# Kernel optimization log

Hardware: AMD Instinct MI355X
Metric: run time of the kernel (lower is better)

Reference implementation:

```python
import jax, jax.numpy as jnp
import numpy as np

B, C, D, K = 65536, 128, 32, 10
EPS = 1e-12


def setup_inputs() -> dict:
    key = jax.random.key(0)
    k1, k2, k3, k4 = jax.random.split(key, 4)
    data = jax.random.normal(k1, (B, D), dtype=jnp.float32)
    mu = jax.random.normal(k2, (C, D), dtype=jnp.float32)
    # S_inv must be symmetric positive definite (inverse covariance per cluster)
    A = 0.1 * jax.random.normal(k3, (C, D, D), dtype=jnp.float32)
    S_inv = jnp.einsum('cij,ckj->cik', A, A) + jnp.eye(D, dtype=jnp.float32)[None]
    # one-hot class assignment per cluster (int32), as stored in the module
    cls = jax.random.randint(k4, (C,), 0, K)
    cluster_labels = jax.nn.one_hot(cls, K, dtype=jnp.int32)
    return {"data": data, "mu": mu, "S_inv": S_inv, "cluster_labels": cluster_labels}


def reference(data, mu, S_inv, cluster_labels):
    # Mahalanobis distance d2[b,c] = (z_b - mu_c)^T S_inv_c (z_b - mu_c),
    # expanded to avoid a [B, C, D] diff tensor.
    zz = data[:, :, None] * data[:, None, :]            # [B, D, D]
    t1 = jnp.einsum('bde,cde->bc', zz, S_inv)           # z' Sinv z
    Sm = jnp.einsum('cde,ce->cd', S_inv, mu)            # [C, D]
    t2 = data @ Sm.T                                    # z' Sinv mu  [B, C]
    t3 = jnp.einsum('cd,cd->c', mu, Sm)                 # mu' Sinv mu [C]
    d2 = t1 - 2.0 * t2 + t3[None, :]                    # [B, C]
    Gamma = jnp.exp(-0.5 * d2)                          # Gaussian activation
    # defuzzify_batch: normalize activations, project through one-hot labels
    norm_gamma = Gamma / (jnp.sum(Gamma, axis=1, keepdims=True) + EPS)
    label_scores = norm_gamma @ cluster_labels.astype(jnp.float32)  # [B, K]
    preds = jnp.argmax(label_scores, axis=1)
    clusters = jnp.argmax(Gamma, axis=1)
    return label_scores, preds, clusters
```

## Files before the change

### kernel.cpp

```cpp
#include <hip/hip_runtime.h>
#include <cmath>

#define B_N 65536
#define C_N 128
#define D_N 32
#define K_N 10
#define EPS_F 1e-12f
#define SCALE_F (-0.72134752044448169f)

#define NKK 45
#define QFRAG_N (4 * NKK * 64 * 8)

typedef _Float16 f16x8 __attribute__((ext_vector_type(8)));
typedef float    f32x16 __attribute__((ext_vector_type(16)));

static constexpr int WDT[NKK] = {
    0,0,0,0,0,  2,2,2,2,  4,4,4,4,  6,6,6,6,  8,8,8,8,
    10,10,10, 12,12,12, 14,14,14, 16,16,16,
    18,18, 20,20, 22,22, 24,24, 26, 28, 30, 32};
static constexpr int WET[NKK] = {
    0,8,16,24,32,  2,10,18,26,  4,12,20,28,  6,14,22,30,  8,16,24,32,
    10,18,26, 12,20,28, 14,22,30, 16,24,32,
    18,26, 20,28, 22,30, 24,32, 26, 28, 30, 32};

__global__ __launch_bounds__(256) void k_prep_sm(const float* __restrict__ S,
                                                 const float* __restrict__ mu,
                                                 float* __restrict__ Sm) {
    int t = blockIdx.x * 256 + threadIdx.x;
    int c = t >> 5;
    int d = t & 31;
    const float* Sr = S + (size_t)c * (D_N * D_N) + (size_t)d * D_N;
    const float* mr = mu + (size_t)c * D_N;
    float a0 = 0.f, a1 = 0.f, a2 = 0.f, a3 = 0.f;
#pragma unroll
    for (int e = 0; e < D_N; e += 4) {
        a0 = fmaf(Sr[e + 0], mr[e + 0], a0);
        a1 = fmaf(Sr[e + 1], mr[e + 1], a1);
        a2 = fmaf(Sr[e + 2], mr[e + 2], a2);
        a3 = fmaf(Sr[e + 3], mr[e + 3], a3);
    }
    Sm[t] = (a0 + a1) + (a2 + a3);
}

__global__ __launch_bounds__(128) void k_prep_misc(const float* __restrict__ mu,
                                                   const float* __restrict__ Sm,
                                                   const int* __restrict__ onehot,
                                                   float* __restrict__ t3,
                                                   int* __restrict__ cls) {
    int c = threadIdx.x;
    const float* mr = mu + (size_t)c * D_N;
    const float* sr = Sm + (size_t)c * D_N;
    float a = 0.f;
#pragma unroll
    for (int d = 0; d < D_N; ++d) a = fmaf(mr[d], sr[d], a);
    t3[c] = a;
    int cl = 0;
#pragma unroll
    for (int k = 0; k < K_N; ++k)
        if (onehot[c * K_N + k] != 0) cl = k;
    cls[c] = cl;
}

__global__ __launch_bounds__(256) void k_packfrag(const float* __restrict__ S,
                                                  const float* __restrict__ Sm,
                                                  const float* __restrict__ t3,
                                                  _Float16* __restrict__ Qh,
                                                  _Float16* __restrict__ Ql) {
    int t = blockIdx.x * 256 + threadIdx.x;
    if (t >= QFRAG_N) return;
    int j    = t & 7;
    int lane = (t >> 3) & 63;
    int rest = t >> 9;
    int kk   = rest % NKK;
    int ct   = rest / NKK;
    int r = 0, base = 0;
    for (;;) {
        int w = (40 - 2 * r) >> 3;
        if (kk < base + w) break;
        base += w; ++r;
    }
    int e0 = 2 * r + 8 * (kk - base);
    int d  = 2 * r + (lane >> 5);
    int e  = e0 + j;
    int c  = ct * 32 + (lane & 31);
    float q = 0.f;
    if (d <= e && e <= 32) {
        float v;
        if (e < 32)      v = S[(size_t)c * (D_N * D_N) + d * D_N + e] * (d == e ? 1.f : 2.f);
        else if (d < 32) v = -2.f * Sm[c * D_N + d];
        else             v = t3[c];
        q = SCALE_F * v;
    }
    _Float16 h = (_Float16)q;
    Qh[t] = h;
    Ql[t] = (_Float16)(q - (float)h);
}

__global__ __launch_bounds__(256, 2) void k_mainv3(const float* __restrict__ data,
                                                   const _Float16* __restrict__ Qhp,
                                                   const _Float16* __restrict__ Qlp,
                                                   const int* __restrict__ clsp,
                                                   float* __restrict__ out) {
    const int lane = threadIdx.x & 63;
    const int wid  = threadIdx.x >> 6;
    const int b0w  = blockIdx.x * 128 + wid * 32;
    const int col  = lane & 31;
    const bool hi  = lane >= 32;

    __shared__ int lcls[C_N];
    if (threadIdx.x < C_N) lcls[threadIdx.x] = clsp[threadIdx.x];

    float y[34];
    {
        const float4* p0 = (const float4*)(data + (size_t)(b0w + col) * D_N);
#pragma unroll
        for (int i = 0; i < 8; ++i) {
            float4 v = p0[i];
            y[4 * i + 0] = v.x; y[4 * i + 1] = v.y;
            y[4 * i + 2] = v.z; y[4 * i + 3] = v.w;
        }
        y[32] = 1.f; y[33] = 0.f;
    }
    __syncthreads();

    f32x16 acc[4];
#pragma unroll
    for (int ct = 0; ct < 4; ++ct)
#pragma unroll
        for (int g = 0; g < 16; ++g) acc[ct][g] = 0.f;

    const f16x8* QH = (const f16x8*)Qhp;
    const f16x8* QL = (const f16x8*)Qlp;

    f16x8 qh[2][4], ql[2][4];
#pragma unroll
    for (int ct = 0; ct < 4; ++ct) {
        qh[0][ct] = QH[(ct * NKK + 0) * 64 + lane];
        ql[0][ct] = QL[(ct * NKK + 0) * 64 + lane];
    }

#pragma unroll
    for (int kk = 0; kk < NKK; ++kk) {
        const int cur = kk & 1;
        const int nxt = cur ^ 1;
        if (kk + 1 < NKK) {
#pragma unroll
            for (int ct = 0; ct < 4; ++ct) {
                qh[nxt][ct] = QH[(ct * NKK + kk + 1) * 64 + lane];
                ql[nxt][ct] = QL[(ct * NKK + kk + 1) * 64 + lane];
            }
        }

        const int dA = WDT[kk];
        const int dB = dA + 1;
        const int e0 = WET[kk];
        const float yd = hi ? y[dB] : y[dA];
        f16x8 ph, pl;
#pragma unroll
        for (int j = 0; j < 8; ++j) {
            const int e = e0 + j;
            float f = (e <= 32) ? yd * y[e] : 0.f;
            _Float16 h = (_Float16)f;
            ph[j] = h;
            pl[j] = (_Float16)(f - (float)h);
        }

#pragma unroll
        for (int ct = 0; ct < 4; ++ct)
            acc[ct] = __builtin_amdgcn_mfma_f32_32x32x16_f16(qh[cur][ct], ph, acc[ct], 0, 0, 0);
#pragma unroll
        for (int ct = 0; ct < 4; ++ct)
            acc[ct] = __builtin_amdgcn_mfma_f32_32x32x16_f16(ql[cur][ct], ph, acc[ct], 0, 0, 0);
#pragma unroll
        for (int ct = 0; ct < 4; ++ct)
            acc[ct] = __builtin_amdgcn_mfma_f32_32x32x16_f16(qh[cur][ct], pl, acc[ct], 0, 0, 0);

        __builtin_amdgcn_s_barrier();
    }

    const float hoff = hi ? 4.f : 0.f;
    const int* lc = lcls + (hi ? 4 : 0);
    float sum = 0.f, gmax = -1.f, gcf = 0.f;
    float a0 = 0, a1 = 0, a2 = 0, a3 = 0, a4 = 0, a5 = 0, a6 = 0, a7 = 0, a8 = 0, a9 = 0;
#pragma unroll
    for (int ct = 0; ct < 4; ++ct) {
        float psum = 0.f;
#pragma unroll
        for (int g = 0; g < 16; ++g) {
            float v = acc[ct][g];
            float gm;
            asm("v_exp_f32 %0, %1" : "=v"(gm) : "v"(v));
            const int cbase = ct * 32 + (g & 3) + 8 * (g >> 2);
            int cl = lc[cbase];
            psum += gm;
            float cf = (float)cbase + hoff;
            if (gm > gmax) { gmax = gm; gcf = cf; }
            a0 += (cl == 0) ? gm : 0.f;
            a1 += (cl == 1) ? gm : 0.f;
            a2 += (cl == 2) ? gm : 0.f;
            a3 += (cl == 3) ? gm : 0.f;
            a4 += (cl == 4) ? gm : 0.f;
            a5 += (cl == 5) ? gm : 0.f;
            a6 += (cl == 6) ? gm : 0.f;
            a7 += (cl == 7) ? gm : 0.f;
            a8 += (cl == 8) ? gm : 0.f;
            a9 += (cl == 9) ? gm : 0.f;
        }
        sum += psum;
    }

    sum += __shfl_xor(sum, 32, 64);
    {
        float om = __shfl_xor(gmax, 32, 64);
        float oc = __shfl_xor(gcf, 32, 64);
        bool take = (om > gmax) || (om == gmax && oc < gcf);
        if (take) { gmax = om; gcf = oc; }
    }
    a0 += __shfl_xor(a0, 32, 64);
    a1 += __shfl_xor(a1, 32, 64);
    a2 += __shfl_xor(a2, 32, 64);
    a3 += __shfl_xor(a3, 32, 64);
    a4 += __shfl_xor(a4, 32, 64);
    a5 += __shfl_xor(a5, 32, 64);
    a6 += __shfl_xor(a6, 32, 64);
    a7 += __shfl_xor(a7, 32, 64);
    a8 += __shfl_xor(a8, 32, 64);
    a9 += __shfl_xor(a9, 32, 64);

    if (!hi) {
        const int b = b0w + col;
        float inv = 1.0f / (sum + EPS_F);
        float ls[K_N] = {a0 * inv, a1 * inv, a2 * inv, a3 * inv, a4 * inv,
                         a5 * inv, a6 * inv, a7 * inv, a8 * inv, a9 * inv};
        float best = -1.f;
        int bk = 0;
#pragma unroll
        for (int k = 0; k < K_N; ++k)
            if (ls[k] > best) { best = ls[k]; bk = k; }
        float2* o2 = (float2*)(out + (size_t)b * K_N);
#pragma unroll
        for (int k2 = 0; k2 < K_N / 2; ++k2)
            o2[k2] = make_float2(ls[2 * k2], ls[2 * k2 + 1]);
        out[(size_t)B_N * K_N + b] = (float)bk;
        out[(size_t)B_N * K_N + B_N + b] = gcf;
    }
}

extern "C" void kernel_launch(void* const* d_in, const int* in_sizes, int n_in,
                              void* d_out, int out_size, void* d_ws, size_t ws_size,
                              hipStream_t stream) {
    const float* data   = (const float*)d_in[0];
    const float* mu     = (const float*)d_in[1];
    const float* S      = (const float*)d_in[2];
    const int*   onehot = (const int*)d_in[3];
    float* out = (float*)d_out;

    _Float16* Qh  = (_Float16*)d_ws;
    _Float16* Ql  = Qh + QFRAG_N;
    float*    Sm  = (float*)(Ql + QFRAG_N);
    float*    t3  = Sm + C_N * D_N;
    int*      cls = (int*)(t3 + C_N);

    hipLaunchKernelGGL(k_prep_sm, dim3((C_N * D_N) / 256), dim3(256), 0, stream,
                       S, mu, Sm);
    hipLaunchKernelGGL(k_prep_misc, dim3(1), dim3(128), 0, stream,
                       mu, Sm, onehot, t3, cls);
    hipLaunchKernelGGL(k_packfrag, dim3((QFRAG_N + 255) / 256), dim3(256), 0, stream,
                       S, Sm, t3, Qh, Ql);
    hipLaunchKernelGGL(k_mainv3, dim3(B_N / 128), dim3(256), 0, stream,
                       data, Qh, Ql, cls, out);
}
```

Before: 127.3 us.

## Fuse prep kernels into one per-cluster kernel and template-unroll main loop

Merges the three preprocessing launches (Sm, t3/labels, fragment packing) into a single kernel with one block per cluster, keeping Sm and t3 in shared memory. This removes two kernel launches and the global round-trips between them. The main kernel's k-loop becomes compile-time template recursion so table lookups are constexpr, and the per-iteration s_barrier is dropped. The fused prep does only 90 active threads per block writing scalar halves, so its stores are less coalesced.

```diff
diff --git a/kernel.cpp b/kernel.cpp
--- a/kernel.cpp
+++ b/kernel.cpp
@@ -23,80 +23,119 @@
     10,18,26, 12,20,28, 14,22,30, 16,24,32,
     18,26, 20,28, 22,30, 24,32, 26, 28, 30, 32};
 
-__global__ __launch_bounds__(256) void k_prep_sm(const float* __restrict__ S,
-                                                 const float* __restrict__ mu,
-                                                 float* __restrict__ Sm) {
-    int t = blockIdx.x * 256 + threadIdx.x;
-    int c = t >> 5;
-    int d = t & 31;
-    const float* Sr = S + (size_t)c * (D_N * D_N) + (size_t)d * D_N;
-    const float* mr = mu + (size_t)c * D_N;
-    float a0 = 0.f, a1 = 0.f, a2 = 0.f, a3 = 0.f;
-#pragma unroll
-    for (int e = 0; e < D_N; e += 4) {
-        a0 = fmaf(Sr[e + 0], mr[e + 0], a0);
-        a1 = fmaf(Sr[e + 1], mr[e + 1], a1);
-        a2 = fmaf(Sr[e + 2], mr[e + 2], a2);
-        a3 = fmaf(Sr[e + 3], mr[e + 3], a3);
-    }
-    Sm[t] = (a0 + a1) + (a2 + a3);
-}
-
-__global__ __launch_bounds__(128) void k_prep_misc(const float* __restrict__ mu,
-                                                   const float* __restrict__ Sm,
-                                                   const int* __restrict__ onehot,
-                                                   float* __restrict__ t3,
-                                                   int* __restrict__ cls) {
-    int c = threadIdx.x;
-    const float* mr = mu + (size_t)c * D_N;
-    const float* sr = Sm + (size_t)c * D_N;
-    float a = 0.f;
-#pragma unroll
-    for (int d = 0; d < D_N; ++d) a = fmaf(mr[d], sr[d], a);
-    t3[c] = a;
-    int cl = 0;
-#pragma unroll
-    for (int k = 0; k < K_N; ++k)
-        if (onehot[c * K_N + k] != 0) cl = k;
-    cls[c] = cl;
-}
-
-__global__ __launch_bounds__(256) void k_packfrag(const float* __restrict__ S,
-                                                  const float* __restrict__ Sm,
-                                                  const float* __restrict__ t3,
-                                                  _Float16* __restrict__ Qh,
-                                                  _Float16* __restrict__ Ql) {
-    int t = blockIdx.x * 256 + threadIdx.x;
-    if (t >= QFRAG_N) return;
-    int j    = t & 7;
-    int lane = (t >> 3) & 63;
-    int rest = t >> 9;
-    int kk   = rest % NKK;
-    int ct   = rest / NKK;
-    int r = 0, base = 0;
-    for (;;) {
-        int w = (40 - 2 * r) >> 3;
-        if (kk < base + w) break;
-        base += w; ++r;
-    }
-    int e0 = 2 * r + 8 * (kk - base);
-    int d  = 2 * r + (lane >> 5);
-    int e  = e0 + j;
-    int c  = ct * 32 + (lane & 31);
-    float q = 0.f;
-    if (d <= e && e <= 32) {
-        float v;
-        if (e < 32)      v = S[(size_t)c * (D_N * D_N) + d * D_N + e] * (d == e ? 1.f : 2.f);
-        else if (d < 32) v = -2.f * Sm[c * D_N + d];
-        else             v = t3[c];
-        q = SCALE_F * v;
-    }
-    _Float16 h = (_Float16)q;
-    Qh[t] = h;
-    Ql[t] = (_Float16)(q - (float)h);
-}
-
-__global__ __launch_bounds__(256, 2) void k_mainv3(const float* __restrict__ data,
+__global__ __launch_bounds__(128) void k_prep(const float* __restrict__ S,
+                                              const float* __restrict__ mu,
+                                              const int* __restrict__ onehot,
+                                              _Float16* __restrict__ Qh,
+                                              _Float16* __restrict__ Ql,
+                                              int* __restrict__ cls) {
+    const int c = blockIdx.x;
+    const int tid = threadIdx.x;
+    __shared__ float sSm[D_N];
+    __shared__ float st3;
+
+    if (tid < D_N) {
+        const float* Sr = S + (size_t)c * (D_N * D_N) + (size_t)tid * D_N;
+        const float* mr = mu + (size_t)c * D_N;
+        float a0 = 0.f, a1 = 0.f;
+#pragma unroll
+        for (int e = 0; e < D_N; e += 2) {
+            a0 = fmaf(Sr[e + 0], mr[e + 0], a0);
+            a1 = fmaf(Sr[e + 1], mr[e + 1], a1);
+        }
+        sSm[tid] = a0 + a1;
+    }
+    __syncthreads();
+    if (tid == 0) {
+        const float* mr = mu + (size_t)c * D_N;
+        float a = 0.f;
+#pragma unroll
+        for (int d = 0; d < D_N; ++d) a = fmaf(mr[d], sSm[d], a);
+        st3 = a;
+        int cl = 0;
+#pragma unroll
+        for (int k = 0; k < K_N; ++k)
+            if (onehot[c * K_N + k] != 0) cl = k;
+        cls[c] = cl;
+    }
+    __syncthreads();
+
+    if (tid < 2 * NKK) {
+        const int kk   = tid >> 1;
+        const int half = tid & 1;
+        const int e0 = WET[kk];
+        const int d  = WDT[kk] + half;
+        const int ct = c >> 5;
+        const size_t base =
+            ((size_t)(ct * NKK + kk) * 64 + half * 32 + (c & 31)) * 8;
+        const float* Sc = S + (size_t)c * (D_N * D_N);
+        for (int j = 0; j < 8; ++j) {
+            const int e = e0 + j;
+            float q = 0.f;
+            if (d <= e && e <= 32) {
+                float v;
+                if (e < 32)      v = Sc[d * D_N + e] * (d == e ? 1.f : 2.f);
+                else if (d < 32) v = -2.f * sSm[d];
+                else             v = st3;
+                q = SCALE_F * v;
+            }
+            _Float16 h = (_Float16)q;
+            Qh[base + j] = h;
+            Ql[base + j] = (_Float16)(q - (float)h);
+        }
+    }
+}
+
+template <int KK>
+__device__ __forceinline__ void kstep(const f16x8* __restrict__ QH,
+                                      const f16x8* __restrict__ QL,
+                                      int lane, bool hi, const float (&y)[34],
+                                      f16x8 (&bh)[2][4], f16x8 (&bl)[2][4],
+                                      f32x16 (&acc)[4]) {
+    constexpr int cur = KK & 1;
+    constexpr int nxt = cur ^ 1;
+    if constexpr (KK + 1 < NKK) {
+#pragma unroll
+        for (int ct = 0; ct < 4; ++ct) {
+            bh[nxt][ct] = QH[(ct * NKK + KK + 1) * 64 + lane];
+            bl[nxt][ct] = QL[(ct * NKK + KK + 1) * 64 + lane];
+        }
+    }
+    constexpr int dA = WDT[KK];
+    constexpr int e0 = WET[KK];
+    const float yd = hi ? y[dA + 1] : y[dA];
+    f16x8 ph, pl;
+#pragma unroll
+    for (int j = 0; j < 8; ++j) {
+        float f = (e0 + j <= 32) ? yd * y[e0 + j] : 0.f;
+        _Float16 h = (_Float16)f;
+        ph[j] = h;
+        pl[j] = (_Float16)(f - (float)h);
+    }
+#pragma unroll
+    for (int ct = 0; ct < 4; ++ct)
+        acc[ct] = __builtin_amdgcn_mfma_f32_32x32x16_f16(bh[cur][ct], ph, acc[ct], 0, 0, 0);
+#pragma unroll
+    for (int ct = 0; ct < 4; ++ct)
+        acc[ct] = __builtin_amdgcn_mfma_f32_32x32x16_f16(bl[cur][ct], ph, acc[ct], 0, 0, 0);
+#pragma unroll
+    for (int ct = 0; ct < 4; ++ct)
+        acc[ct] = __builtin_amdgcn_mfma_f32_32x32x16_f16(bh[cur][ct], pl, acc[ct], 0, 0, 0);
+}
+
+template <int KK>
+__device__ __forceinline__ void loop_from(const f16x8* __restrict__ QH,
+                                          const f16x8* __restrict__ QL,
+                                          int lane, bool hi, const float (&y)[34],
+                                          f16x8 (&bh)[2][4], f16x8 (&bl)[2][4],
+                                          f32x16 (&acc)[4]) {
+    if constexpr (KK < NKK) {
+        kstep<KK>(QH, QL, lane, hi, y, bh, bl, acc);
+        loop_from<KK + 1>(QH, QL, lane, hi, y, bh, bl, acc);
+    }
+}
+
+__global__ __launch_bounds__(256, 2) void k_mainv4(const float* __restrict__ data,
                                                    const _Float16* __restrict__ Qhp,
                                                    const _Float16* __restrict__ Qlp,
                                                    const int* __restrict__ clsp,
@@ -132,51 +171,14 @@
     const f16x8* QH = (const f16x8*)Qhp;
     const f16x8* QL = (const f16x8*)Qlp;
 
-    f16x8 qh[2][4], ql[2][4];
+    f16x8 bh[2][4], bl[2][4];
 #pragma unroll
     for (int ct = 0; ct < 4; ++ct) {
-        qh[0][ct] = QH[(ct * NKK + 0) * 64 + lane];
-        ql[0][ct] = QL[(ct * NKK + 0) * 64 + lane];
-    }
-
-#pragma unroll
-    for (int kk = 0; kk < NKK; ++kk) {
-        const int cur = kk & 1;
-        const int nxt = cur ^ 1;
-        if (kk + 1 < NKK) {
-#pragma unroll
-            for (int ct = 0; ct < 4; ++ct) {
-                qh[nxt][ct] = QH[(ct * NKK + kk + 1) * 64 + lane];
-                ql[nxt][ct] = QL[(ct * NKK + kk + 1) * 64 + lane];
-            }
-        }
-
-        const int dA = WDT[kk];
-        const int dB = dA + 1;
-        const int e0 = WET[kk];
-        const float yd = hi ? y[dB] : y[dA];
-        f16x8 ph, pl;
-#pragma unroll
-        for (int j = 0; j < 8; ++j) {
-            const int e = e0 + j;
-            float f = (e <= 32) ? yd * y[e] : 0.f;
-            _Float16 h = (_Float16)f;
-            ph[j] = h;
-            pl[j] = (_Float16)(f - (float)h);
-        }
-
-#pragma unroll
-        for (int ct = 0; ct < 4; ++ct)
-            acc[ct] = __builtin_amdgcn_mfma_f32_32x32x16_f16(qh[cur][ct], ph, acc[ct], 0, 0, 0);
-#pragma unroll
-        for (int ct = 0; ct < 4; ++ct)
-            acc[ct] = __builtin_amdgcn_mfma_f32_32x32x16_f16(ql[cur][ct], ph, acc[ct], 0, 0, 0);
-#pragma unroll
-        for (int ct = 0; ct < 4; ++ct)
-            acc[ct] = __builtin_amdgcn_mfma_f32_32x32x16_f16(qh[cur][ct], pl, acc[ct], 0, 0, 0);
-
-        __builtin_amdgcn_s_barrier();
-    }
+        bh[0][ct] = QH[(ct * NKK + 0) * 64 + lane];
+        bl[0][ct] = QL[(ct * NKK + 0) * 64 + lane];
+    }
+
+    loop_from<0>(QH, QL, lane, hi, y, bh, bl, acc);
 
     const float hoff = hi ? 4.f : 0.f;
     const int* lc = lcls + (hi ? 4 : 0);
@@ -257,16 +259,10 @@
 
     _Float16* Qh  = (_Float16*)d_ws;
     _Float16* Ql  = Qh + QFRAG_N;
-    float*    Sm  = (float*)(Ql + QFRAG_N);
-    float*    t3  = Sm + C_N * D_N;
-    int*      cls = (int*)(t3 + C_N);
-
-    hipLaunchKernelGGL(k_prep_sm, dim3((C_N * D_N) / 256), dim3(256), 0, stream,
-                       S, mu, Sm);
-    hipLaunchKernelGGL(k_prep_misc, dim3(1), dim3(128), 0, stream,
-                       mu, Sm, onehot, t3, cls);
-    hipLaunchKernelGGL(k_packfrag, dim3((QFRAG_N + 255) / 256), dim3(256), 0, stream,
-                       S, Sm, t3, Qh, Ql);
-    hipLaunchKernelGGL(k_mainv3, dim3(B_N / 128), dim3(256), 0, stream,
+    int*      cls = (int*)(Ql + QFRAG_N);
+
+    hipLaunchKernelGGL(k_prep, dim3(C_N), dim3(128), 0, stream,
+                       S, mu, onehot, Qh, Ql, cls);
+    hipLaunchKernelGGL(k_mainv4, dim3(B_N / 128), dim3(256), 0, stream,
                        data, Qh, Ql, cls, out);
 }
```

After: 126.0 us. About the same (-1.0%).
